# Performance work log

Measured on AMD Instinct MI355X. Metric: run time of the kernel, lower is better.

The kernel has to match this reference:

```python
import jax, jax.numpy as jnp
import numpy as np

B, S, D = 2, 2048, 2048
H, KV, HD = 8, 2, 256
EPS = 1e-6
WINDOW = 512
ROPE_THETA = 1000000.0
NEG = -1e9


def setup_inputs() -> dict:
    key = jax.random.key(0)
    ks = jax.random.split(key, 6)
    hidden_states = jax.random.normal(ks[0], (B, S, D), dtype=jnp.float32)
    # rotary tables: [S, HD//2] freqs tiled to [B, S, HD]
    inv_freq = 1.0 / (ROPE_THETA ** (np.arange(0, HD, 2, dtype=np.float32) / HD))
    pos = np.arange(S, dtype=np.float32)
    freqs = np.outer(pos, inv_freq)                      # [S, HD/2]
    emb = np.concatenate([freqs, freqs], axis=-1)        # [S, HD]
    cos = jnp.broadcast_to(jnp.asarray(np.cos(emb))[None], (B, S, HD))
    sin = jnp.broadcast_to(jnp.asarray(np.sin(emb))[None], (B, S, HD))
    # causal sliding-window additive mask: allow k<=q and q-k < WINDOW
    q_idx = np.arange(S)[:, None]
    k_idx = np.arange(S)[None, :]
    allowed = (k_idx <= q_idx) & (q_idx - k_idx < WINDOW)
    attention_mask = jnp.asarray(np.where(allowed, 0.0, NEG).astype(np.float32))[None, None]
    sc = 0.02
    wq = jax.random.normal(ks[1], (D, H * HD), dtype=jnp.float32) * sc
    wk = jax.random.normal(ks[2], (D, KV * HD), dtype=jnp.float32) * sc
    wv = jax.random.normal(ks[3], (D, KV * HD), dtype=jnp.float32) * sc
    wo = jax.random.normal(ks[4], (H * HD, D), dtype=jnp.float32) * sc
    q_norm_w = jnp.ones((HD,), dtype=jnp.float32)
    k_norm_w = jnp.ones((HD,), dtype=jnp.float32)
    return dict(hidden_states=hidden_states, cos=cos, sin=sin,
                attention_mask=attention_mask, wq=wq, wk=wk, wv=wv, wo=wo,
                q_norm_w=q_norm_w, k_norm_w=k_norm_w)


def _rms_norm(x, w):
    xf = x.astype(jnp.float32)
    y = xf * jax.lax.rsqrt(jnp.mean(xf * xf, axis=-1, keepdims=True) + EPS)
    return (y * w).astype(x.dtype)


def _apply_rope(x, cos, sin):
    # x: [B, S, N, HD]; cos/sin: [B, S, HD] -> unsqueeze at dim 2
    c = cos[:, :, None, :]
    s = sin[:, :, None, :]
    x1, x2 = jnp.split(x, 2, axis=-1)
    rot = jnp.concatenate([-x2, x1], axis=-1)
    return x * c + rot * s


def reference(hidden_states, cos, sin, attention_mask, wq, wk, wv, wo,
              q_norm_w, k_norm_w):
    b, s, _ = hidden_states.shape
    n_rep = H // KV
    q = (hidden_states @ wq).reshape(b, s, H, HD)
    q = _apply_rope(_rms_norm(q, q_norm_w), cos, sin).transpose(0, 2, 1, 3)   # [B,H,S,HD]
    k = (hidden_states @ wk).reshape(b, s, KV, HD)
    k = _apply_rope(_rms_norm(k, k_norm_w), cos, sin).transpose(0, 2, 1, 3)   # [B,KV,S,HD]
    v = (hidden_states @ wv).reshape(b, s, KV, HD)
    v = _rms_norm(v, jnp.float32(1.0)).transpose(0, 2, 1, 3)                  # [B,KV,S,HD]
    k = jnp.repeat(k, n_rep, axis=1)  # GQA repeat_kv -> [B,H,S,HD]
    v = jnp.repeat(v, n_rep, axis=1)
    # Gemma3n uses scaling = 1.0 (QK-RMSNorm replaces 1/sqrt(d))
    scores = jnp.einsum('bhqd,bhkd->bhqk', q, k) + attention_mask[:, :, :, :s]
    probs = jax.nn.softmax(scores.astype(jnp.float32), axis=-1).astype(q.dtype)
    out = jnp.einsum('bhqk,bhkd->bhqd', probs, v)
    out = out.transpose(0, 2, 1, 3).reshape(b, s, H * HD)
    return out @ wo
```

## Files before the change

### kernel.cpp

```cpp
#include <hip/hip_runtime.h>
#include <hip/hip_bf16.h>
#include <hip/hip_fp16.h>

#define B_ 2
#define S_ 2048
#define D_ 2048
#define H_ 8
#define KV_ 2
#define HD_ 256
#define WINDOW_ 512
#define EPS_ 1e-6f
#define MASKV_ -30000.0f

typedef _Float16 f16;
typedef _Float16 half8 __attribute__((ext_vector_type(8)));
typedef _Float16 half2v __attribute__((ext_vector_type(2)));
typedef float floatx4 __attribute__((ext_vector_type(4)));

#define GLOAD_LDS16(g, l)                                                        \
    __builtin_amdgcn_global_load_lds(                                            \
        (const __attribute__((address_space(1))) unsigned int*)(g),              \
        (__attribute__((address_space(3))) unsigned int*)(l), 16, 0, 0)

__global__ __launch_bounds__(256) void prep(const float* __restrict__ x,
                                            const float* __restrict__ wq,
                                            const float* __restrict__ wk,
                                            const float* __restrict__ wv,
                                            const float* __restrict__ wo,
                                            f16* __restrict__ xh,
                                            f16* __restrict__ BT,
                                            f16* __restrict__ woT) {
    int bid = blockIdx.x;
    const int t = threadIdx.x;
    if (bid < 8192) {
        const int i = bid * 256 + t;
        float4 v = ((const float4*)x)[i];
        typedef _Float16 half4v __attribute__((ext_vector_type(4)));
        half4v hv = {(f16)v.x, (f16)v.y, (f16)v.z, (f16)v.w};
        ((half4v*)xh)[i] = hv;
        return;
    }
    bid -= 8192;
    const float* src;
    f16* dst;
    int C, bx, by;
    if (bid < 4096) {
        src = wq; dst = BT; C = 2048; bx = bid & 63; by = bid >> 6;
    } else if (bid < 5120) {
        const int b2 = bid - 4096;
        src = wk; dst = BT + (size_t)2048 * 2048; C = 512; bx = b2 & 15; by = b2 >> 4;
    } else if (bid < 6144) {
        const int b2 = bid - 5120;
        src = wv; dst = BT + (size_t)2560 * 2048; C = 512; bx = b2 & 15; by = b2 >> 4;
    } else {
        const int b2 = bid - 6144;
        src = wo; dst = woT; C = 2048; bx = b2 & 63; by = b2 >> 6;
    }
    __shared__ float tile[32][33];
    const int tx = t & 31, ty = t >> 5;
    const int c0 = bx * 32, r0 = by * 32;
#pragma unroll
    for (int i = 0; i < 4; ++i)
        tile[ty + i * 8][tx] = src[(size_t)(r0 + ty + i * 8) * C + c0 + tx];
    __syncthreads();
#pragma unroll
    for (int i = 0; i < 4; ++i)
        dst[(size_t)(c0 + ty + i * 8) * 2048 + r0 + tx] = (f16)tile[tx][ty + i * 8];
}

template <typename OutT>
__global__ __launch_bounds__(256) void gemm_f16(const f16* __restrict__ A,
                                                const f16* __restrict__ BT,
                                                OutT* __restrict__ C,
                                                int M, int N, int K) {
    __shared__ __align__(16) f16 sA[128 * 32];
    __shared__ __align__(16) f16 sB[128 * 32];

    const int t = threadIdx.x;
    const int lane = t & 63;
    const int w = t >> 6;
    const int i16 = lane & 15, q4 = lane >> 4;
    const int m0 = blockIdx.y * 128, n0 = blockIdx.x * 128;
    const int mw = (w & 1) * 64, nw = (w >> 1) * 64;

    floatx4 acc[16];
#pragma unroll
    for (int i = 0; i < 16; ++i) acc[i] = (floatx4){0.f, 0.f, 0.f, 0.f};

    const int srow = w * 32 + (lane >> 2);
    const int sgp = lane & 3;

    for (int k0 = 0; k0 < K; k0 += 32) {
#pragma unroll
        for (int c = 0; c < 2; ++c) {
            const int chunk = w * 2 + c;
            const int row = srow + c * 16;
            const int g = (sgp - (row >> 1)) & 3;
            GLOAD_LDS16(A + (size_t)(m0 + row) * K + k0 + g * 8,
                        sA + chunk * 512 + lane * 8);
            GLOAD_LDS16(BT + (size_t)(n0 + row) * K + k0 + g * 8,
                        sB + chunk * 512 + lane * 8);
        }
        __syncthreads();

        half8 af[4], bf[4];
#pragma unroll
        for (int mi = 0; mi < 4; ++mi) {
            const int row = mw + mi * 16 + i16;
            const int gp = (q4 + (row >> 1)) & 3;
            af[mi] = *(const half8*)(sA + row * 32 + gp * 8);
        }
#pragma unroll
        for (int ni = 0; ni < 4; ++ni) {
            const int row = nw + ni * 16 + i16;
            const int gp = (q4 + (row >> 1)) & 3;
            bf[ni] = *(const half8*)(sB + row * 32 + gp * 8);
        }
#pragma unroll
        for (int mi = 0; mi < 4; ++mi)
#pragma unroll
            for (int ni = 0; ni < 4; ++ni)
                acc[mi * 4 + ni] = __builtin_amdgcn_mfma_f32_16x16x32_f16(
                    af[mi], bf[ni], acc[mi * 4 + ni], 0, 0, 0);
        __syncthreads();
    }

#pragma unroll
    for (int mi = 0; mi < 4; ++mi)
#pragma unroll
        for (int ni = 0; ni < 4; ++ni)
#pragma unroll
            for (int r = 0; r < 4; ++r) {
                const int row = m0 + mw + mi * 16 + q4 * 4 + r;
                const int col = n0 + nw + ni * 16 + i16;
                C[(size_t)row * N + col] = (OutT)acc[mi * 4 + ni][r];
            }
}

__global__ __launch_bounds__(256) void norm_rope_f16(
    f16* __restrict__ QKVh, f16* __restrict__ Kh, f16* __restrict__ Vt,
    const float* __restrict__ cosb, const float* __restrict__ sinb,
    const float* __restrict__ qw, const float* __restrict__ kw) {
    const int gid = blockIdx.x * 256 + threadIdx.x;
    const int wid = gid >> 6, lane = gid & 63;
    const int nq = B_ * S_ * H_;
    const int nk = B_ * S_ * KV_;
    const int d0 = lane * 2;

    if (wid < nq) {
        const int b = wid / (S_ * H_);
        const int r = wid % (S_ * H_);
        const int s = r / H_, h = r % H_;
        f16* p = QKVh + (size_t)(b * S_ + s) * 3072 + h * HD_;
        half2v lo = *(const half2v*)(p + d0);
        half2v hi = *(const half2v*)(p + 128 + d0);
        float x0 = (float)lo[0], x1 = (float)lo[1], x2 = (float)hi[0], x3 = (float)hi[1];
        float ss = x0 * x0 + x1 * x1 + x2 * x2 + x3 * x3;
#pragma unroll
        for (int off = 32; off >= 1; off >>= 1) ss += __shfl_xor(ss, off);
        const float inv = rsqrtf(ss * (1.0f / HD_) + EPS_);
        float2 wlo = *(const float2*)(qw + d0), whi = *(const float2*)(qw + 128 + d0);
        float y0 = x0 * inv * wlo.x, y1 = x1 * inv * wlo.y;
        float y2 = x2 * inv * whi.x, y3 = x3 * inv * whi.y;
        const float* cb = cosb + (size_t)(b * S_ + s) * HD_;
        const float* sb = sinb + (size_t)(b * S_ + s) * HD_;
        float2 clo = *(const float2*)(cb + d0), chi = *(const float2*)(cb + 128 + d0);
        float2 slo = *(const float2*)(sb + d0), shi = *(const float2*)(sb + 128 + d0);
        half2v olo = {(f16)(y0 * clo.x - y2 * slo.x), (f16)(y1 * clo.y - y3 * slo.y)};
        half2v ohi = {(f16)(y2 * chi.x + y0 * shi.x), (f16)(y3 * chi.y + y1 * shi.y)};
        *(half2v*)(p + d0) = olo;
        *(half2v*)(p + 128 + d0) = ohi;
    } else if (wid < nq + nk) {
        const int idx = wid - nq;
        const int b = idx / (S_ * KV_);
        const int r = idx % (S_ * KV_);
        const int s = r / KV_, kv = r % KV_;
        const f16* p = QKVh + (size_t)(b * S_ + s) * 3072 + 2048 + kv * HD_;
        half2v lo = *(const half2v*)(p + d0);
        half2v hi = *(const half2v*)(p + 128 + d0);
        float x0 = (float)lo[0], x1 = (float)lo[1], x2 = (float)hi[0], x3 = (float)hi[1];
        float ss = x0 * x0 + x1 * x1 + x2 * x2 + x3 * x3;
#pragma unroll
        for (int off = 32; off >= 1; off >>= 1) ss += __shfl_xor(ss, off);
        const float inv = rsqrtf(ss * (1.0f / HD_) + EPS_);
        float2 wlo = *(const float2*)(kw + d0), whi = *(const float2*)(kw + 128 + d0);
        float y0 = x0 * inv * wlo.x, y1 = x1 * inv * wlo.y;
        float y2 = x2 * inv * whi.x, y3 = x3 * inv * whi.y;
        const float* cb = cosb + (size_t)(b * S_ + s) * HD_;
        const float* sb = sinb + (size_t)(b * S_ + s) * HD_;
        float2 clo = *(const float2*)(cb + d0), chi = *(const float2*)(cb + 128 + d0);
        float2 slo = *(const float2*)(sb + d0), shi = *(const float2*)(sb + 128 + d0);
        half2v olo = {(f16)(y0 * clo.x - y2 * slo.x), (f16)(y1 * clo.y - y3 * slo.y)};
        half2v ohi = {(f16)(y2 * chi.x + y0 * shi.x), (f16)(y3 * chi.y + y1 * shi.y)};
        f16* d = Kh + ((size_t)(b * KV_ + kv) * S_ + s) * HD_;
        *(half2v*)(d + d0) = olo;
        *(half2v*)(d + 128 + d0) = ohi;
    } else {
        const int idx = wid - nq - nk;
        const int b = idx / (S_ * KV_);
        const int r = idx % (S_ * KV_);
        const int s = r / KV_, kv = r % KV_;
        const f16* p = QKVh + (size_t)(b * S_ + s) * 3072 + 2560 + kv * HD_;
        half2v lo = *(const half2v*)(p + d0);
        half2v hi = *(const half2v*)(p + 128 + d0);
        float x0 = (float)lo[0], x1 = (float)lo[1], x2 = (float)hi[0], x3 = (float)hi[1];
        float ss = x0 * x0 + x1 * x1 + x2 * x2 + x3 * x3;
#pragma unroll
        for (int off = 32; off >= 1; off >>= 1) ss += __shfl_xor(ss, off);
        const float inv = rsqrtf(ss * (1.0f / HD_) + EPS_);
        f16* d = Vt + (size_t)(b * KV_ + kv) * HD_ * S_;
        d[(size_t)d0 * S_ + s] = (f16)(x0 * inv);
        d[(size_t)(d0 + 1) * S_ + s] = (f16)(x1 * inv);
        d[(size_t)(d0 + 128) * S_ + s] = (f16)(x2 * inv);
        d[(size_t)(d0 + 129) * S_ + s] = (f16)(x3 * inv);
    }
}

__global__ __launch_bounds__(512, 2) void attn_mfma(const f16* __restrict__ QKVh,
                                                    const f16* __restrict__ Kh,
                                                    const f16* __restrict__ Vt,
                                                    f16* __restrict__ attnh) {
    __shared__ __align__(16) f16 sK[2][64 * 256];
    __shared__ __align__(16) f16 sV[2][256 * 64];
    __shared__ __align__(16) f16 sP[8][16 * 72];

    const int qt = blockIdx.x, h = blockIdx.y, b = blockIdx.z;
    const int kvh = h / (H_ / KV_);
    const int t = threadIdx.x, lane = t & 63, w = t >> 6;
    const int i16 = lane & 15, q4 = lane >> 4;

    const int qrow = qt * 128 + w * 16 + i16;
    const f16* qbase = QKVh + (size_t)(b * S_ + qrow) * 3072 + h * HD_ + q4 * 8;
    half8 qf[8];
#pragma unroll
    for (int kk = 0; kk < 8; ++kk) qf[kk] = *(const half8*)(qbase + kk * 32);

    floatx4 o[16];
#pragma unroll
    for (int i = 0; i < 16; ++i) o[i] = (floatx4){0.f, 0.f, 0.f, 0.f};
    float mrow[4] = {-1e30f, -1e30f, -1e30f, -1e30f};
    float lrow[4] = {0.f, 0.f, 0.f, 0.f};

    const size_t kbase = (size_t)(b * KV_ + kvh) * S_ * HD_;
    const size_t vbase = (size_t)(b * KV_ + kvh) * HD_ * S_;
    const int srow0 = qt * 128 + w * 16 + q4 * 4;

    const int kt_lo = (2 * qt - 8) > 0 ? (2 * qt - 8) : 0;
    const int kt_hi = 2 * qt + 1;
    const int s_lo_w = qt * 128 + w * 16;
    int ktw_lo = (s_lo_w - (WINDOW_ - 1)) >> 6;
    if (ktw_lo < kt_lo) ktw_lo = kt_lo;
    const int ktw_hi = (s_lo_w + 15) >> 6;

    auto stage = [&](int kt, int buf) {
#pragma unroll
        for (int c = 0; c < 4; ++c) {
            const int chunk = w * 4 + c;
            const int keyl = chunk * 2 + (lane >> 5);
            const int g = (lane & 31) ^ (keyl & 31);
            GLOAD_LDS16(Kh + kbase + (size_t)(kt * 64 + keyl) * HD_ + g * 8,
                        sK[buf] + chunk * 512 + lane * 8);
            const int diml = chunk * 8 + (lane >> 3);
            const int g2 = (lane & 7) ^ (diml & 7);
            GLOAD_LDS16(Vt + vbase + (size_t)diml * S_ + kt * 64 + g2 * 8,
                        sV[buf] + chunk * 512 + lane * 8);
        }
    };

    stage(kt_lo, 0);
    int cur = 0;
    for (int kt = kt_lo; kt <= kt_hi; ++kt, cur ^= 1) {
        __syncthreads();
        if (kt < kt_hi) stage(kt + 1, cur ^ 1);
        if (kt < ktw_lo || kt > ktw_hi) continue;

        const f16* sKc = sK[cur];
        const f16* sVc = sV[cur];

        floatx4 sc[4];
#pragma unroll
        for (int nt = 0; nt < 4; ++nt) sc[nt] = (floatx4){0.f, 0.f, 0.f, 0.f};
#pragma unroll
        for (int ks = 0; ks < 8; ++ks)
#pragma unroll
            for (int nt = 0; nt < 4; ++nt) {
                const int keyl = nt * 16 + i16;
                const int gp = (ks * 4 + q4) ^ (keyl & 31);
                half8 kf = *(const half8*)(sKc + keyl * 256 + gp * 8);
                sc[nt] = __builtin_amdgcn_mfma_f32_16x16x32_f16(qf[ks], kf, sc[nt], 0, 0, 0);
            }

#pragma unroll
        for (int r = 0; r < 4; ++r) {
            const int s = srow0 + r;
            float mx = -1e30f;
#pragma unroll
            for (int nt = 0; nt < 4; ++nt) {
                const int j = kt * 64 + nt * 16 + i16;
                const bool valid = (j <= s) && (s - j < WINDOW_);
                const float v = valid ? sc[nt][r] : MASKV_;
                sc[nt][r] = v;
                mx = fmaxf(mx, v);
            }
#pragma unroll
            for (int off = 1; off < 16; off <<= 1) mx = fmaxf(mx, __shfl_xor(mx, off));
            const float mnew = fmaxf(mrow[r], mx);
            const float alpha = __expf(mrow[r] - mnew);
            mrow[r] = mnew;
            float rs = 0.f;
#pragma unroll
            for (int nt = 0; nt < 4; ++nt) {
                const float p = __expf(sc[nt][r] - mnew);
                sc[nt][r] = p;
                rs += p;
            }
#pragma unroll
            for (int off = 1; off < 16; off <<= 1) rs += __shfl_xor(rs, off);
            lrow[r] = lrow[r] * alpha + rs;
#pragma unroll
            for (int nt2 = 0; nt2 < 16; ++nt2) o[nt2][r] *= alpha;
        }

        f16* sPw = sP[w];
#pragma unroll
        for (int nt = 0; nt < 4; ++nt)
#pragma unroll
            for (int r = 0; r < 4; ++r)
                sPw[(q4 * 4 + r) * 72 + nt * 16 + i16] = (f16)sc[nt][r];
        asm volatile("s_waitcnt lgkmcnt(0)" ::: "memory");

#pragma unroll
        for (int kt2 = 0; kt2 < 2; ++kt2) {
            half8 pf = *(const half8*)(sPw + i16 * 72 + kt2 * 32 + q4 * 8);
#pragma unroll
            for (int nt2 = 0; nt2 < 16; ++nt2) {
                const int dim = nt2 * 16 + i16;
                const int gp = (kt2 * 4 + q4) ^ (dim & 7);
                half8 vf = *(const half8*)(sVc + dim * 64 + gp * 8);
                o[nt2] = __builtin_amdgcn_mfma_f32_16x16x32_f16(pf, vf, o[nt2], 0, 0, 0);
            }
        }
    }

    float inv[4];
#pragma unroll
    for (int r = 0; r < 4; ++r) inv[r] = 1.0f / lrow[r];
    f16* ob = attnh + (size_t)(b * S_ + qt * 128 + w * 16) * (H_ * HD_) + h * HD_;
#pragma unroll
    for (int nt2 = 0; nt2 < 16; ++nt2)
#pragma unroll
        for (int r = 0; r < 4; ++r)
            ob[(size_t)(q4 * 4 + r) * (H_ * HD_) + nt2 * 16 + i16] =
                (f16)(o[nt2][r] * inv[r]);
}

extern "C" void kernel_launch(void* const* d_in, const int* in_sizes, int n_in,
                              void* d_out, int out_size, void* d_ws, size_t ws_size,
                              hipStream_t stream) {
    const float* x    = (const float*)d_in[0];
    const float* cosb = (const float*)d_in[1];
    const float* sinb = (const float*)d_in[2];
    const float* wq = (const float*)d_in[4];
    const float* wk = (const float*)d_in[5];
    const float* wv = (const float*)d_in[6];
    const float* wo = (const float*)d_in[7];
    const float* qw = (const float*)d_in[8];
    const float* kw = (const float*)d_in[9];
    float* out = (float*)d_out;

    f16* ws = (f16*)d_ws;
    f16* xh    = ws;
    f16* BT    = xh + 8388608;
    f16* woT   = BT + 6291456;
    f16* QKVh  = woT + 4194304;
    f16* Kh    = QKVh + 12582912;
    f16* Vt    = Kh + 2097152;
    f16* attnh = xh;

    const int M = B_ * S_;

    prep<<<18432, 256, 0, stream>>>(x, wq, wk, wv, wo, xh, BT, woT);

    gemm_f16<f16><<<dim3(24, 32), 256, 0, stream>>>(xh, BT, QKVh, M, 3072, D_);

    norm_rope_f16<<<(B_ * S_ * (H_ + 2 * KV_) * 64) / 256, 256, 0, stream>>>(
        QKVh, Kh, Vt, cosb, sinb, qw, kw);

    attn_mfma<<<dim3(S_ / 128, H_, B_), 512, 0, stream>>>(QKVh, Kh, Vt, attnh);

    gemm_f16<float><<<dim3(16, 32), 256, 0, stream>>>(attnh, woT, out, M, D_, H_ * HD_);
}
```

Baseline: 333.8 us.

## Single-buffer attention LDS for higher occupancy and transpose V via shared memory

The V normalization path now stages 64 rows in shared memory and writes the transposed Vt with coalesced rows instead of strided scalar stores. The attention kernel drops K/V double buffering and shrinks the P scratch to cut LDS use, raising launch bounds to 4 blocks per CU. P·V is now processed in two halves to reduce live registers. The trade is losing the prefetch overlap of the next K/V tile and adding an extra barrier per tile, in exchange for more resident waves hiding latency.

```diff
diff --git a/kernel.cpp b/kernel.cpp
--- a/kernel.cpp
+++ b/kernel.cpp
@@ -15,6 +15,7 @@
 typedef _Float16 f16;
 typedef _Float16 half8 __attribute__((ext_vector_type(8)));
 typedef _Float16 half2v __attribute__((ext_vector_type(2)));
+typedef _Float16 half4v __attribute__((ext_vector_type(4)));
 typedef float floatx4 __attribute__((ext_vector_type(4)));
 
 #define GLOAD_LDS16(g, l)                                                        \
@@ -35,7 +36,6 @@
     if (bid < 8192) {
         const int i = bid * 256 + t;
         float4 v = ((const float4*)x)[i];
-        typedef _Float16 half4v __attribute__((ext_vector_type(4)));
         half4v hv = {(f16)v.x, (f16)v.y, (f16)v.z, (f16)v.w};
         ((half4v*)xh)[i] = hv;
         return;
@@ -137,21 +137,82 @@
             }
 }
 
+#define NRB_ ((B_ * S_ * (H_ + KV_)) / 4)
+
 __global__ __launch_bounds__(256) void norm_rope_f16(
     f16* __restrict__ QKVh, f16* __restrict__ Kh, f16* __restrict__ Vt,
     const float* __restrict__ cosb, const float* __restrict__ sinb,
     const float* __restrict__ qw, const float* __restrict__ kw) {
-    const int gid = blockIdx.x * 256 + threadIdx.x;
-    const int wid = gid >> 6, lane = gid & 63;
-    const int nq = B_ * S_ * H_;
-    const int nk = B_ * S_ * KV_;
-    const int d0 = lane * 2;
-
-    if (wid < nq) {
-        const int b = wid / (S_ * H_);
-        const int r = wid % (S_ * H_);
-        const int s = r / H_, h = r % H_;
-        f16* p = QKVh + (size_t)(b * S_ + s) * 3072 + h * HD_;
+    __shared__ f16 vt[64][266];
+
+    const int w = threadIdx.x >> 6, lane = threadIdx.x & 63;
+
+    if (blockIdx.x < NRB_) {
+        const int wid = blockIdx.x * 4 + w;
+        const int nq = B_ * S_ * H_;
+        const int d0 = lane * 2;
+
+        if (wid < nq) {
+            const int b = wid / (S_ * H_);
+            const int r = wid % (S_ * H_);
+            const int s = r / H_, h = r % H_;
+            f16* p = QKVh + (size_t)(b * S_ + s) * 3072 + h * HD_;
+            half2v lo = *(const half2v*)(p + d0);
+            half2v hi = *(const half2v*)(p + 128 + d0);
+            float x0 = (float)lo[0], x1 = (float)lo[1], x2 = (float)hi[0], x3 = (float)hi[1];
+            float ss = x0 * x0 + x1 * x1 + x2 * x2 + x3 * x3;
+#pragma unroll
+            for (int off = 32; off >= 1; off >>= 1) ss += __shfl_xor(ss, off);
+            const float inv = rsqrtf(ss * (1.0f / HD_) + EPS_);
+            float2 wlo = *(const float2*)(qw + d0), whi = *(const float2*)(qw + 128 + d0);
+            float y0 = x0 * inv * wlo.x, y1 = x1 * inv * wlo.y;
+            float y2 = x2 * inv * whi.x, y3 = x3 * inv * whi.y;
+            const float* cb = cosb + (size_t)(b * S_ + s) * HD_;
+            const float* sb = sinb + (size_t)(b * S_ + s) * HD_;
+            float2 clo = *(const float2*)(cb + d0), chi = *(const float2*)(cb + 128 + d0);
+            float2 slo = *(const float2*)(sb + d0), shi = *(const float2*)(sb + 128 + d0);
+            half2v olo = {(f16)(y0 * clo.x - y2 * slo.x), (f16)(y1 * clo.y - y3 * slo.y)};
+            half2v ohi = {(f16)(y2 * chi.x + y0 * shi.x), (f16)(y3 * chi.y + y1 * shi.y)};
+            *(half2v*)(p + d0) = olo;
+            *(half2v*)(p + 128 + d0) = ohi;
+        } else {
+            const int idx = wid - nq;
+            const int b = idx / (S_ * KV_);
+            const int r = idx % (S_ * KV_);
+            const int s = r / KV_, kv = r % KV_;
+            const f16* p = QKVh + (size_t)(b * S_ + s) * 3072 + 2048 + kv * HD_;
+            half2v lo = *(const half2v*)(p + d0);
+            half2v hi = *(const half2v*)(p + 128 + d0);
+            float x0 = (float)lo[0], x1 = (float)lo[1], x2 = (float)hi[0], x3 = (float)hi[1];
+            float ss = x0 * x0 + x1 * x1 + x2 * x2 + x3 * x3;
+#pragma unroll
+            for (int off = 32; off >= 1; off >>= 1) ss += __shfl_xor(ss, off);
+            const float inv = rsqrtf(ss * (1.0f / HD_) + EPS_);
+            float2 wlo = *(const float2*)(kw + d0), whi = *(const float2*)(kw + 128 + d0);
+            float y0 = x0 * inv * wlo.x, y1 = x1 * inv * wlo.y;
+            float y2 = x2 * inv * whi.x, y3 = x3 * inv * whi.y;
+            const float* cb = cosb + (size_t)(b * S_ + s) * HD_;
+            const float* sb = sinb + (size_t)(b * S_ + s) * HD_;
+            float2 clo = *(const float2*)(cb + d0), chi = *(const float2*)(cb + 128 + d0);
+            float2 slo = *(const float2*)(sb + d0), shi = *(const float2*)(sb + 128 + d0);
+            half2v olo = {(f16)(y0 * clo.x - y2 * slo.x), (f16)(y1 * clo.y - y3 * slo.y)};
+            half2v ohi = {(f16)(y2 * chi.x + y0 * shi.x), (f16)(y3 * chi.y + y1 * shi.y)};
+            f16* d = Kh + ((size_t)(b * KV_ + kv) * S_ + s) * HD_;
+            *(half2v*)(d + d0) = olo;
+            *(half2v*)(d + 128 + d0) = ohi;
+        }
+        return;
+    }
+
+    const int vb = blockIdx.x - NRB_;
+    const int s0 = (vb & 31) * 64;
+    const int kv = (vb >> 5) & 1;
+    const int b  = vb >> 6;
+
+    for (int r = 0; r < 16; ++r) {
+        const int sl = w * 16 + r;
+        const f16* p = QKVh + (size_t)(b * S_ + s0 + sl) * 3072 + 2560 + kv * HD_;
+        const int d0 = lane * 2;
         half2v lo = *(const half2v*)(p + d0);
         half2v hi = *(const half2v*)(p + 128 + d0);
         float x0 = (float)lo[0], x1 = (float)lo[1], x2 = (float)hi[0], x3 = (float)hi[1];
@@ -159,70 +220,26 @@
 #pragma unroll
         for (int off = 32; off >= 1; off >>= 1) ss += __shfl_xor(ss, off);
         const float inv = rsqrtf(ss * (1.0f / HD_) + EPS_);
-        float2 wlo = *(const float2*)(qw + d0), whi = *(const float2*)(qw + 128 + d0);
-        float y0 = x0 * inv * wlo.x, y1 = x1 * inv * wlo.y;
-        float y2 = x2 * inv * whi.x, y3 = x3 * inv * whi.y;
-        const float* cb = cosb + (size_t)(b * S_ + s) * HD_;
-        const float* sb = sinb + (size_t)(b * S_ + s) * HD_;
-        float2 clo = *(const float2*)(cb + d0), chi = *(const float2*)(cb + 128 + d0);
-        float2 slo = *(const float2*)(sb + d0), shi = *(const float2*)(sb + 128 + d0);
-        half2v olo = {(f16)(y0 * clo.x - y2 * slo.x), (f16)(y1 * clo.y - y3 * slo.y)};
-        half2v ohi = {(f16)(y2 * chi.x + y0 * shi.x), (f16)(y3 * chi.y + y1 * shi.y)};
-        *(half2v*)(p + d0) = olo;
-        *(half2v*)(p + 128 + d0) = ohi;
-    } else if (wid < nq + nk) {
-        const int idx = wid - nq;
-        const int b = idx / (S_ * KV_);
-        const int r = idx % (S_ * KV_);
-        const int s = r / KV_, kv = r % KV_;
-        const f16* p = QKVh + (size_t)(b * S_ + s) * 3072 + 2048 + kv * HD_;
-        half2v lo = *(const half2v*)(p + d0);
-        half2v hi = *(const half2v*)(p + 128 + d0);
-        float x0 = (float)lo[0], x1 = (float)lo[1], x2 = (float)hi[0], x3 = (float)hi[1];
-        float ss = x0 * x0 + x1 * x1 + x2 * x2 + x3 * x3;
-#pragma unroll
-        for (int off = 32; off >= 1; off >>= 1) ss += __shfl_xor(ss, off);
-        const float inv = rsqrtf(ss * (1.0f / HD_) + EPS_);
-        float2 wlo = *(const float2*)(kw + d0), whi = *(const float2*)(kw + 128 + d0);
-        float y0 = x0 * inv * wlo.x, y1 = x1 * inv * wlo.y;
-        float y2 = x2 * inv * whi.x, y3 = x3 * inv * whi.y;
-        const float* cb = cosb + (size_t)(b * S_ + s) * HD_;
-        const float* sb = sinb + (size_t)(b * S_ + s) * HD_;
-        float2 clo = *(const float2*)(cb + d0), chi = *(const float2*)(cb + 128 + d0);
-        float2 slo = *(const float2*)(sb + d0), shi = *(const float2*)(sb + 128 + d0);
-        half2v olo = {(f16)(y0 * clo.x - y2 * slo.x), (f16)(y1 * clo.y - y3 * slo.y)};
-        half2v ohi = {(f16)(y2 * chi.x + y0 * shi.x), (f16)(y3 * chi.y + y1 * shi.y)};
-        f16* d = Kh + ((size_t)(b * KV_ + kv) * S_ + s) * HD_;
-        *(half2v*)(d + d0) = olo;
-        *(half2v*)(d + 128 + d0) = ohi;
-    } else {
-        const int idx = wid - nq - nk;
-        const int b = idx / (S_ * KV_);
-        const int r = idx % (S_ * KV_);
-        const int s = r / KV_, kv = r % KV_;
-        const f16* p = QKVh + (size_t)(b * S_ + s) * 3072 + 2560 + kv * HD_;
-        half2v lo = *(const half2v*)(p + d0);
-        half2v hi = *(const half2v*)(p + 128 + d0);
-        float x0 = (float)lo[0], x1 = (float)lo[1], x2 = (float)hi[0], x3 = (float)hi[1];
-        float ss = x0 * x0 + x1 * x1 + x2 * x2 + x3 * x3;
-#pragma unroll
-        for (int off = 32; off >= 1; off >>= 1) ss += __shfl_xor(ss, off);
-        const float inv = rsqrtf(ss * (1.0f / HD_) + EPS_);
-        f16* d = Vt + (size_t)(b * KV_ + kv) * HD_ * S_;
-        d[(size_t)d0 * S_ + s] = (f16)(x0 * inv);
-        d[(size_t)(d0 + 1) * S_ + s] = (f16)(x1 * inv);
-        d[(size_t)(d0 + 128) * S_ + s] = (f16)(x2 * inv);
-        d[(size_t)(d0 + 129) * S_ + s] = (f16)(x3 * inv);
+        half2v olo = {(f16)(x0 * inv), (f16)(x1 * inv)};
+        half2v ohi = {(f16)(x2 * inv), (f16)(x3 * inv)};
+        *(half2v*)&vt[sl][d0] = olo;
+        *(half2v*)&vt[sl][128 + d0] = ohi;
+    }
+    __syncthreads();
+    f16* dst = Vt + (size_t)(b * KV_ + kv) * HD_ * S_;
+    for (int i = 0; i < 64; ++i) {
+        const int dd = w * 64 + i;
+        dst[(size_t)dd * S_ + s0 + lane] = vt[lane][dd];
     }
 }
 
-__global__ __launch_bounds__(512, 2) void attn_mfma(const f16* __restrict__ QKVh,
+__global__ __launch_bounds__(512, 4) void attn_mfma(const f16* __restrict__ QKVh,
                                                     const f16* __restrict__ Kh,
                                                     const f16* __restrict__ Vt,
                                                     f16* __restrict__ attnh) {
-    __shared__ __align__(16) f16 sK[2][64 * 256];
-    __shared__ __align__(16) f16 sV[2][256 * 64];
-    __shared__ __align__(16) f16 sP[8][16 * 72];
+    __shared__ __align__(16) f16 sK[64 * 256];
+    __shared__ __align__(16) f16 sV[256 * 64];
+    __shared__ __align__(16) f16 sP[8][16 * 40];
 
     const int qt = blockIdx.x, h = blockIdx.y, b = blockIdx.z;
     const int kvh = h / (H_ / KV_);
@@ -252,94 +269,87 @@
     if (ktw_lo < kt_lo) ktw_lo = kt_lo;
     const int ktw_hi = (s_lo_w + 15) >> 6;
 
-    auto stage = [&](int kt, int buf) {
+    for (int kt = kt_lo; kt <= kt_hi; ++kt) {
 #pragma unroll
         for (int c = 0; c < 4; ++c) {
             const int chunk = w * 4 + c;
             const int keyl = chunk * 2 + (lane >> 5);
             const int g = (lane & 31) ^ (keyl & 31);
             GLOAD_LDS16(Kh + kbase + (size_t)(kt * 64 + keyl) * HD_ + g * 8,
-                        sK[buf] + chunk * 512 + lane * 8);
+                        sK + chunk * 512 + lane * 8);
             const int diml = chunk * 8 + (lane >> 3);
             const int g2 = (lane & 7) ^ (diml & 7);
             GLOAD_LDS16(Vt + vbase + (size_t)diml * S_ + kt * 64 + g2 * 8,
-                        sV[buf] + chunk * 512 + lane * 8);
-        }
-    };
-
-    stage(kt_lo, 0);
-    int cur = 0;
-    for (int kt = kt_lo; kt <= kt_hi; ++kt, cur ^= 1) {
+                        sV + chunk * 512 + lane * 8);
+        }
         __syncthreads();
-        if (kt < kt_hi) stage(kt + 1, cur ^ 1);
-        if (kt < ktw_lo || kt > ktw_hi) continue;
-
-        const f16* sKc = sK[cur];
-        const f16* sVc = sV[cur];
-
-        floatx4 sc[4];
-#pragma unroll
-        for (int nt = 0; nt < 4; ++nt) sc[nt] = (floatx4){0.f, 0.f, 0.f, 0.f};
-#pragma unroll
-        for (int ks = 0; ks < 8; ++ks)
+
+        if (kt >= ktw_lo && kt <= ktw_hi) {
+            floatx4 sc[4];
 #pragma unroll
             for (int nt = 0; nt < 4; ++nt) {
+                floatx4 a = (floatx4){0.f, 0.f, 0.f, 0.f};
                 const int keyl = nt * 16 + i16;
-                const int gp = (ks * 4 + q4) ^ (keyl & 31);
-                half8 kf = *(const half8*)(sKc + keyl * 256 + gp * 8);
-                sc[nt] = __builtin_amdgcn_mfma_f32_16x16x32_f16(qf[ks], kf, sc[nt], 0, 0, 0);
+#pragma unroll
+                for (int ks = 0; ks < 8; ++ks) {
+                    const int gp = (ks * 4 + q4) ^ (keyl & 31);
+                    half8 kf = *(const half8*)(sK + keyl * 256 + gp * 8);
+                    a = __builtin_amdgcn_mfma_f32_16x16x32_f16(qf[ks], kf, a, 0, 0, 0);
+                }
+                sc[nt] = a;
             }
 
 #pragma unroll
-        for (int r = 0; r < 4; ++r) {
-            const int s = srow0 + r;
-            float mx = -1e30f;
-#pragma unroll
-            for (int nt = 0; nt < 4; ++nt) {
-                const int j = kt * 64 + nt * 16 + i16;
-                const bool valid = (j <= s) && (s - j < WINDOW_);
-                const float v = valid ? sc[nt][r] : MASKV_;
-                sc[nt][r] = v;
-                mx = fmaxf(mx, v);
+            for (int r = 0; r < 4; ++r) {
+                const int s = srow0 + r;
+                float mx = -1e30f;
+#pragma unroll
+                for (int nt = 0; nt < 4; ++nt) {
+                    const int j = kt * 64 + nt * 16 + i16;
+                    const bool valid = (j <= s) && (s - j < WINDOW_);
+                    const float v = valid ? sc[nt][r] : MASKV_;
+                    sc[nt][r] = v;
+                    mx = fmaxf(mx, v);
+                }
+#pragma unroll
+                for (int off = 1; off < 16; off <<= 1) mx = fmaxf(mx, __shfl_xor(mx, off));
+                const float mnew = fmaxf(mrow[r], mx);
+                const float alpha = __expf(mrow[r] - mnew);
+                mrow[r] = mnew;
+                float rs = 0.f;
+#pragma unroll
+                for (int nt = 0; nt < 4; ++nt) {
+                    const float p = __expf(sc[nt][r] - mnew);
+                    sc[nt][r] = p;
+                    rs += p;
+                }
+#pragma unroll
+                for (int off = 1; off < 16; off <<= 1) rs += __shfl_xor(rs, off);
+                lrow[r] = lrow[r] * alpha + rs;
+#pragma unroll
+                for (int nt2 = 0; nt2 < 16; ++nt2) o[nt2][r] *= alpha;
             }
-#pragma unroll
-            for (int off = 1; off < 16; off <<= 1) mx = fmaxf(mx, __shfl_xor(mx, off));
-            const float mnew = fmaxf(mrow[r], mx);
-            const float alpha = __expf(mrow[r] - mnew);
-            mrow[r] = mnew;
-            float rs = 0.f;
-#pragma unroll
-            for (int nt = 0; nt < 4; ++nt) {
-                const float p = __expf(sc[nt][r] - mnew);
-                sc[nt][r] = p;
-                rs += p;
+
+            f16* sPw = sP[w];
+#pragma unroll
+            for (int hf = 0; hf < 2; ++hf) {
+#pragma unroll
+                for (int nt = 0; nt < 2; ++nt)
+#pragma unroll
+                    for (int r = 0; r < 4; ++r)
+                        sPw[(q4 * 4 + r) * 40 + nt * 16 + i16] = (f16)sc[hf * 2 + nt][r];
+                asm volatile("s_waitcnt lgkmcnt(0)" ::: "memory");
+                half8 pf = *(const half8*)(sPw + i16 * 40 + q4 * 8);
+#pragma unroll
+                for (int nt2 = 0; nt2 < 16; ++nt2) {
+                    const int dim = nt2 * 16 + i16;
+                    const int gp = (hf * 4 + q4) ^ (dim & 7);
+                    half8 vf = *(const half8*)(sV + dim * 64 + gp * 8);
+                    o[nt2] = __builtin_amdgcn_mfma_f32_16x16x32_f16(pf, vf, o[nt2], 0, 0, 0);
+                }
             }
-#pragma unroll
-            for (int off = 1; off < 16; off <<= 1) rs += __shfl_xor(rs, off);
-            lrow[r] = lrow[r] * alpha + rs;
-#pragma unroll
-            for (int nt2 = 0; nt2 < 16; ++nt2) o[nt2][r] *= alpha;
-        }
-
-        f16* sPw = sP[w];
-#pragma unroll
-        for (int nt = 0; nt < 4; ++nt)
-#pragma unroll
-            for (int r = 0; r < 4; ++r)
-                sPw[(q4 * 4 + r) * 72 + nt * 16 + i16] = (f16)sc[nt][r];
-        asm volatile("s_waitcnt lgkmcnt(0)" ::: "memory");
-
-#pragma unroll
-        for (int kt2 = 0; kt2 < 2; ++kt2) {
-            half8 pf = *(const half8*)(sPw + i16 * 72 + kt2 * 32 + q4 * 8);
-#pragma unroll
-            for (int nt2 = 0; nt2 < 16; ++nt2) {
-                const int dim = nt2 * 16 + i16;
-                const int gp = (kt2 * 4 + q4) ^ (dim & 7);
-                half8 vf = *(const half8*)(sVc + dim * 64 + gp * 8);
-                o[nt2] = __builtin_amdgcn_mfma_f32_16x16x32_f16(pf, vf, o[nt2], 0, 0, 0);
-            }
-        }
+        }
+        __syncthreads();
     }
 
     float inv[4];
@@ -383,8 +393,7 @@
 
     gemm_f16<f16><<<dim3(24, 32), 256, 0, stream>>>(xh, BT, QKVh, M, 3072, D_);
 
-    norm_rope_f16<<<(B_ * S_ * (H_ + 2 * KV_) * 64) / 256, 256, 0, stream>>>(
-        QKVh, Kh, Vt, cosb, sinb, qw, kw);
+    norm_rope_f16<<<NRB_ + 128, 256, 0, stream>>>(QKVh, Kh, Vt, cosb, sinb, qw, kw);
 
     attn_mfma<<<dim3(S_ / 128, H_, B_), 512, 0, stream>>>(QKVh, Kh, Vt, attnh);
 
```

Measured after the change: 428.5 us. 28.4% more time.
